# Optimization experiments

Hardware: AMD Instinct MI355X
Metric: run time of the kernel (lower is better)

Reference implementation:

```python
import jax, jax.numpy as jnp
import numpy as np

EMBED_DIM = 512
NUM_HEADS = 8
HEAD_DIM = EMBED_DIM // NUM_HEADS
EDGE_DIM = 16
B, N = 2, 2048


def setup_inputs() -> dict:
    key = jax.random.key(0)
    ks = jax.random.split(key, 16)
    s = 1.0 / np.sqrt(EMBED_DIM)
    inp = {
        "x": jax.random.normal(ks[0], (B, N, EMBED_DIM), dtype=jnp.float32),
        "adjacency": jax.random.uniform(ks[1], (B, N, N), dtype=jnp.float32),
        # torch.nn.Linear stores weight as (out, in); we keep that convention
        "Wq": jax.random.uniform(ks[2], (EMBED_DIM, EMBED_DIM), minval=-s, maxval=s),
        "bq": jax.random.uniform(ks[3], (EMBED_DIM,), minval=-s, maxval=s),
        "Wk": jax.random.uniform(ks[4], (EMBED_DIM, EMBED_DIM), minval=-s, maxval=s),
        "bk": jax.random.uniform(ks[5], (EMBED_DIM,), minval=-s, maxval=s),
        "Wv": jax.random.uniform(ks[6], (EMBED_DIM, EMBED_DIM), minval=-s, maxval=s),
        "bv": jax.random.uniform(ks[7], (EMBED_DIM,), minval=-s, maxval=s),
        "Wo": jax.random.uniform(ks[8], (EMBED_DIM, EMBED_DIM), minval=-s, maxval=s),
        "bo": jax.random.uniform(ks[9], (EMBED_DIM,), minval=-s, maxval=s),
        # edge MLP: Linear(1 -> edge_dim) then Linear(edge_dim -> num_heads)
        "We1": jax.random.uniform(ks[10], (EDGE_DIM, 1), minval=-1.0, maxval=1.0),
        "be1": jax.random.uniform(ks[11], (EDGE_DIM,), minval=-1.0, maxval=1.0),
        "We2": jax.random.uniform(ks[12], (NUM_HEADS, EDGE_DIM), minval=-0.25, maxval=0.25),
        "be2": jax.random.uniform(ks[13], (NUM_HEADS,), minval=-0.25, maxval=0.25),
        "edge_bias": jnp.zeros((NUM_HEADS,), dtype=jnp.float32),
    }
    return inp


def reference(x, adjacency, Wq, bq, Wk, bk, Wv, bv, Wo, bo, We1, be1, We2, be2, edge_bias):
    b, n, _ = x.shape
    scale = HEAD_DIM ** (-0.5)

    def split_heads(t):  # (b, n, E) -> (b, H, n, d)
        return t.reshape(b, n, NUM_HEADS, HEAD_DIM).transpose(0, 2, 1, 3)

    q = split_heads(x @ Wq.T + bq)
    k = split_heads(x @ Wk.T + bk)
    v = split_heads(x @ Wv.T + bv)

    # (b, H, n, n)
    attn_scores = jnp.einsum('bhid,bhjd->bhij', q, k) * scale

    # edge MLP applied pointwise to each adjacency entry: 1 -> edge_dim -> num_heads
    # hidden: (b, n, n, edge_dim)
    hidden = jax.nn.relu(adjacency[..., None] * We1[:, 0] + be1)
    edge_attn = jnp.einsum('bijE,hE->bhij', hidden, We2) + be2[None, :, None, None]

    boost = adjacency[:, None, :, :] * edge_bias[None, :, None, None]
    attn_scores = attn_scores + edge_attn + boost

    attn_probs = jax.nn.softmax(attn_scores, axis=-1)
    out = jnp.einsum('bhij,bhjd->bhid', attn_probs, v)
    out = out.transpose(0, 2, 1, 3).reshape(b, n, EMBED_DIM)
    out = out @ Wo.T + bo
    return out
```

## Files before the change

### kernel.cpp

```cpp
#include <hip/hip_runtime.h>
#include <stdint.h>


#define SEQ 2048
#define EMB 512
#define NH  8
#define HD  64
#define NB  2
#define L2E 1.4426950408889634f

typedef unsigned int   u32;
typedef unsigned short u16;
typedef u32   u32x4  __attribute__((ext_vector_type(4)));
typedef float f32x4  __attribute__((ext_vector_type(4)));
typedef __bf16 bf16x8 __attribute__((ext_vector_type(8)));

#define MFMA16(a, b, c) __builtin_amdgcn_mfma_f32_16x16x32_bf16((a), (b), (c), 0, 0, 0)

static __device__ __forceinline__ u16 f2bf(float f) {
  return __builtin_bit_cast(u16, (__bf16)f);
}
static __device__ __forceinline__ u32 pack2(float a, float b) {
  return (u32)f2bf(a) | ((u32)f2bf(b) << 16);
}
static __device__ __forceinline__ bf16x8 ldfrag(const u16* p) {
  return __builtin_bit_cast(bf16x8, *(const u32x4*)p);
}
static __device__ __forceinline__ void glds16(const u16* g, u16* l) {
  __builtin_amdgcn_global_load_lds(
      (const __attribute__((address_space(1))) u32*)(const void*)g,
      (__attribute__((address_space(3))) u32*)(void*)l, 16, 0, 0);
}


__global__ void prep_kernel(const float* __restrict__ x,
                            const float* __restrict__ Wq, const float* __restrict__ Wk,
                            const float* __restrict__ Wv, const float* __restrict__ Wo,
                            const float* __restrict__ We1, const float* __restrict__ be1,
                            const float* __restrict__ We2, const float* __restrict__ be2,
                            const float* __restrict__ ebias,
                            u16* __restrict__ xb, u16* __restrict__ wqkv,
                            u16* __restrict__ wob, float* __restrict__ co) {
  const int blk = blockIdx.x, tid = threadIdx.x;
  if (blk < 2048) {
    int i = (blk * 256 + tid) * 4;
    float4 v = *(const float4*)(x + i);
    *(uint2*)(xb + i) = make_uint2(pack2(v.x, v.y), pack2(v.z, v.w));
  } else if (blk < 3072) {
    int i = ((blk - 2048) * 256 + tid) * 4;
    int m = i >> 18;
    int off = i & 262143;
    const float* src = (m == 0) ? Wq : ((m == 1) ? Wk : ((m == 2) ? Wv : Wo));
    u16* dst = (m < 3) ? (wqkv + (size_t)m * 262144) : wob;
    float4 v = *(const float4*)(src + off);
    *(uint2*)(dst + off) = make_uint2(pack2(v.x, v.y), pack2(v.z, v.w));
  } else {
    const int e = tid & 15, h = tid >> 4;
    if (tid < 128) {
      co[49 + e * 8 + h] = 0.0f;
      if (h == 0) { co[17 + e] = 0.0f; co[33 + e] = 0.0f; }
    }
    __syncthreads();
    if (tid < 128) {
      float w1 = We1[e], b1 = be1[e], w2 = We2[h * 16 + e];
      float u0 = b1, u1 = w1 + b1;
      bool on  = (u0 >= 0.0f) && (u1 >= 0.0f);
      bool off = (u0 <= 0.0f) && (u1 <= 0.0f);
      bool crossing = (!on) && (!off);
      float ca = on ? (w2 * b1) : (crossing ? 0.5f * w2 * b1 : 0.0f);
      float cb = on ? (w2 * w1) : (crossing ? 0.5f * w2 * w1 : 0.0f);
      #pragma unroll
      for (int d = 1; d < 16; d <<= 1) { ca += __shfl_xor(ca, d); cb += __shfl_xor(cb, d); }
      if (e == 0) { co[h] = (be2[h] + ca) * L2E; co[8 + h] = (ebias[h] + cb) * L2E; }
      unsigned long long msk = __ballot(crossing);
      int midx = __popcll(msk & 0xFFFFull & ((1ull << e) - 1ull));
      int mcnt = __popcll(msk & 0xFFFFull);
      if (crossing) {
        co[49 + midx * 8 + h] = 0.5f * w2 * L2E;
        if (h == 0) { co[17 + midx] = w1; co[33 + midx] = b1; }
      }
      if (tid == 0) ((int*)co)[16] = mcnt;
    }
  }
}

#define LDA 40
__global__ __launch_bounds__(256) void gemm_qkv_kernel(
    const u16* __restrict__ A, const u16* __restrict__ Bm,
    const float* __restrict__ bq, const float* __restrict__ bk, const float* __restrict__ bv,
    u16* __restrict__ qh, u16* __restrict__ ksw, u16* __restrict__ vsw)
{
  __shared__ u16 sm[64 * LDA + 128 * LDA];
  u16* As = sm;
  u16* Bs = sm + 64 * LDA;
  const int tid = threadIdx.x;
  const int lane = tid & 63, w = tid >> 6;
  const int q = lane >> 4, l15 = lane & 15;
  const int m0 = blockIdx.y * 64;
  const int n0 = blockIdx.x * 128;

  f32x4 acc[4][2];
  f32x4 zero = {0.f, 0.f, 0.f, 0.f};
  #pragma unroll
  for (int i = 0; i < 4; i++) { acc[i][0] = zero; acc[i][1] = zero; }

  const bool isA = tid < 128;
  const int arow_ = tid >> 1, ahalf = tid & 1;
  const int brow = tid - 128;
  const u16* ga = A  + (size_t)(m0 + arow_) * EMB + ahalf * 16;
  const u16* gb = Bm + (size_t)(n0 + brow) * EMB;
  u16* la = &As[arow_ * LDA + ahalf * 16];
  u16* lb = &Bs[brow * LDA];

  u32x4 p0, p1, p2, p3;
  if (isA) {
    p0 = *(const u32x4*)(ga); p1 = *(const u32x4*)(ga + 8); ga += 32;
  } else {
    p0 = *(const u32x4*)(gb);      p1 = *(const u32x4*)(gb + 8);
    p2 = *(const u32x4*)(gb + 16); p3 = *(const u32x4*)(gb + 24); gb += 32;
  }

  for (int k0 = 0; k0 < EMB; k0 += 32) {
    __syncthreads();
    if (isA) { *(u32x4*)(la) = p0; *(u32x4*)(la + 8) = p1; }
    else {
      *(u32x4*)(lb)      = p0; *(u32x4*)(lb + 8)  = p1;
      *(u32x4*)(lb + 16) = p2; *(u32x4*)(lb + 24) = p3;
    }
    __syncthreads();
    if (k0 + 32 < EMB) {
      if (isA) { p0 = *(const u32x4*)(ga); p1 = *(const u32x4*)(ga + 8); ga += 32; }
      else {
        p0 = *(const u32x4*)(gb);      p1 = *(const u32x4*)(gb + 8);
        p2 = *(const u32x4*)(gb + 16); p3 = *(const u32x4*)(gb + 24); gb += 32;
      }
    }
    bf16x8 af[4], bfr[2];
    #pragma unroll
    for (int mi = 0; mi < 4; mi++)
      af[mi] = ldfrag(&As[(mi*16 + l15) * LDA + q*8]);
    #pragma unroll
    for (int ni = 0; ni < 2; ni++)
      bfr[ni] = ldfrag(&Bs[(w*32 + ni*16 + l15) * LDA + q*8]);
    #pragma unroll
    for (int mi = 0; mi < 4; mi++)
      #pragma unroll
      for (int ni = 0; ni < 2; ni++)
        acc[mi][ni] = MFMA16(af[mi], bfr[ni], acc[mi][ni]);
  }

  const int mat = n0 >> 9;
  const float* bias = (mat == 0) ? bq : ((mat == 1) ? bk : bv);
  const float mul = (mat == 0) ? 0.125f * L2E : 1.0f;
  const int b_ = m0 >> 11;
  const int nbase = m0 & 2047;

  #pragma unroll
  for (int p = 0; p < 2; p++) {
    __syncthreads();
    if ((w >> 1) == p) {
      #pragma unroll
      for (int ni = 0; ni < 2; ni++) {
        const int dd = (w & 1) * 32 + ni * 16 + l15;
        const float bsv = bias[(n0 & 511) + (w * 32 + ni * 16 + l15)];
        #pragma unroll
        for (int mi = 0; mi < 4; mi++) {
          #pragma unroll
          for (int r = 0; r < 4; r++) {
            const int nr = mi * 16 + q * 4 + r;
            const float val = (acc[mi][ni][r] + bsv) * mul;
            int idx;
            if (mat == 0)      idx = nr * 64 + dd;
            else if (mat == 1) idx = (nr >> 4) * 1024 + ((dd >> 5) << 9)
                                   + ((((dd >> 3) & 3) * 16 + (nr & 15)) << 3) + (dd & 7);
            else               idx = ((dd >> 4) << 10) + (((nr >> 5) & 1) << 9)
                                   + ((((nr >> 3) & 3) * 16 + (dd & 15)) << 3) + (nr & 7);
            sm[idx] = f2bf(val);
          }
        }
      }
    }
    __syncthreads();
    const int hh = ((n0 & 511) >> 6) + p;
    u16* gdst;
    if (mat == 0)      gdst = qh  + ((size_t)(b_ * NH + hh) * SEQ + nbase) * HD;
    else if (mat == 1) gdst = ksw + (size_t)(b_ * NH + hh) * 131072 + (nbase >> 4) * 1024;
    else               gdst = vsw + (size_t)(b_ * NH + hh) * 131072 + (nbase >> 6) * 4096;
    *(u32x4*)(gdst + tid * 16)     = *(const u32x4*)(sm + tid * 16);
    *(u32x4*)(gdst + tid * 16 + 8) = *(const u32x4*)(sm + tid * 16 + 8);
  }
}

__global__ __launch_bounds__(256) void gemm_out_kernel(
    const u16* __restrict__ A, const u16* __restrict__ Bm,
    const float* __restrict__ bo, float* __restrict__ out)
{
  __shared__ u16 As[64 * LDA];
  __shared__ u16 Bs[64 * LDA];
  const int tid = threadIdx.x;
  const int lane = tid & 63, w = tid >> 6;
  const int q = lane >> 4, l15 = lane & 15;
  const int m0 = blockIdx.y * 64;
  const int n0 = blockIdx.x * 64;

  f32x4 acc[4];
  f32x4 zero = {0.f, 0.f, 0.f, 0.f};
  #pragma unroll
  for (int i = 0; i < 4; i++) acc[i] = zero;

  const bool isA = tid < 128;
  const int row = isA ? (tid >> 1) : ((tid - 128) >> 1);
  const int half = tid & 1;
  const u16* g = (isA ? A + (size_t)(m0 + row) * EMB : Bm + (size_t)(n0 + row) * EMB)
               + half * 16;
  u16* l = (isA ? &As[row * LDA] : &Bs[row * LDA]) + half * 16;

  u32x4 p0 = *(const u32x4*)(g);
  u32x4 p1 = *(const u32x4*)(g + 8);
  g += 32;

  for (int k0 = 0; k0 < EMB; k0 += 32) {
    __syncthreads();
    *(u32x4*)(l) = p0; *(u32x4*)(l + 8) = p1;
    __syncthreads();
    if (k0 + 32 < EMB) {
      p0 = *(const u32x4*)(g); p1 = *(const u32x4*)(g + 8); g += 32;
    }
    bf16x8 af[4], bfr;
    #pragma unroll
    for (int mi = 0; mi < 4; mi++)
      af[mi] = ldfrag(&As[(mi*16 + l15) * LDA + q*8]);
    bfr = ldfrag(&Bs[(w*16 + l15) * LDA + q*8]);
    #pragma unroll
    for (int mi = 0; mi < 4; mi++)
      acc[mi] = MFMA16(af[mi], bfr, acc[mi]);
  }

  int col = n0 + w*16 + l15;
  float bsv = bo[col];
  #pragma unroll
  for (int mi = 0; mi < 4; mi++) {
    int rowb = m0 + mi*16 + q*4;
    #pragma unroll
    for (int r = 0; r < 4; r++)
      out[(size_t)(rowb + r) * EMB + col] = acc[mi][r] + bsv;
  }
}

template<int MT>
struct FlashCtx {
  const u16 *kgp, *vgp;
  const float* arow;
  bf16x8 qf0, qf1;
  float Ah, Bh;
  float ctr[MT], dtr[MT], wtr[MT];
  int lane, w, q, l15;
};

template<int MT>
static __device__ __forceinline__ void flash_stage(const FlashCtx<MT>& c,
                                                   u16* Kb, u16* Vb, int it) {
  const int o = c.w * 1024 + c.lane * 8;
  const u16* kg = c.kgp + it * 4096;
  const u16* vg = c.vgp + it * 4096;
  glds16(kg + o,       Kb + o);
  glds16(kg + o + 512, Kb + o + 512);
  glds16(vg + o,       Vb + o);
  glds16(vg + o + 512, Vb + o + 512);
}

template<int MT>
static __device__ __forceinline__ void flash_iter(
    const FlashCtx<MT>& c, int it, u16* Kb, u16* Vb, u16* nKb, u16* nVb,
    u16* psw, float4* avc, float4* avn, f32x4* O, float& lsum)
{
  __syncthreads();
  if (it + 1 < 32) flash_stage(c, nKb, nVb, it + 1);
  const int nx = (it + 1 < 32) ? it + 1 : 31;
  #pragma unroll
  for (int jt = 0; jt < 4; jt++)
    avn[jt] = *(const float4*)(c.arow + nx * 64 + jt * 16);
  __builtin_amdgcn_sched_barrier(0);

  f32x4 zero = {0.f, 0.f, 0.f, 0.f};
  const int lo = c.lane * 8;

  f32x4 S[4];
  #pragma unroll
  for (int jt = 0; jt < 4; jt++) {
    bf16x8 kf0 = ldfrag(Kb + jt * 1024 + lo);
    bf16x8 kf1 = ldfrag(Kb + jt * 1024 + 512 + lo);
    f32x4 s = MFMA16(kf0, c.qf0, zero);
    S[jt] = MFMA16(kf1, c.qf1, s);
  }

  #pragma unroll
  for (int half = 0; half < 2; half++) {
    #pragma unroll
    for (int jj = 0; jj < 2; jj++) {
      const int jt = half * 2 + jj;
      float p[4];
      #pragma unroll
      for (int r = 0; r < 4; r++) {
        float a = ((const float*)&avc[jt])[r];
        float e = fmaf(a, c.Bh, c.Ah);
        #pragma unroll
        for (int t = 0; t < MT; t++)
          e = fmaf(fabsf(fmaf(a, c.ctr[t], c.dtr[t])), c.wtr[t], e);
        p[r] = __builtin_amdgcn_exp2f(S[jt][r] + e);
        lsum += p[r];
      }
      *(uint2*)(psw + c.l15 * 72 + jt * 16 + c.q * 4) =
          make_uint2(pack2(p[0], p[1]), pack2(p[2], p[3]));
    }
    bf16x8 pf = ldfrag(psw + c.l15 * 72 + half * 32 + c.q * 8);
    #pragma unroll
    for (int dt = 0; dt < 4; dt++) {
      bf16x8 vf = ldfrag(Vb + dt * 1024 + half * 512 + lo);
      O[dt] = MFMA16(vf, pf, O[dt]);
    }
  }
}

template<int MT>
__device__ __forceinline__ void flash_body(
    u16* Kb0, u16* Kb1, u16* Vb0, u16* Vb1, u16* Pb,
    const u16* __restrict__ qh, const u16* __restrict__ ksw, const u16* __restrict__ vsw,
    const float* __restrict__ adj, const float* __restrict__ coeff, u16* __restrict__ om)
{
  const int tid = threadIdx.x, lane = tid & 63, w = tid >> 6;
  const int q = lane >> 4, l15 = lane & 15;
  const int i0 = blockIdx.x * 64;
  const int h = blockIdx.y, b = blockIdx.z;
  const int bh = b * NH + h;
  const int iw = i0 + w * 16;

  FlashCtx<MT> c;
  c.lane = lane; c.w = w; c.q = q; c.l15 = l15;
  c.Ah = coeff[h]; c.Bh = coeff[8 + h];
  #pragma unroll
  for (int t = 0; t < MT; t++) {
    c.ctr[t] = coeff[17 + t];
    c.dtr[t] = coeff[33 + t];
    c.wtr[t] = coeff[49 + t * 8 + h];
  }
  const u16* qrow = qh + ((size_t)bh * SEQ + iw + l15) * HD;
  c.qf0 = ldfrag(qrow + q * 8);
  c.qf1 = ldfrag(qrow + 32 + q * 8);
  c.kgp = ksw + (size_t)bh * 131072;
  c.vgp = vsw + (size_t)bh * 131072;
  c.arow = adj + ((size_t)b * SEQ + iw + l15) * SEQ + q * 4;

  f32x4 O[4];
  f32x4 zero = {0.f, 0.f, 0.f, 0.f};
  #pragma unroll
  for (int dt = 0; dt < 4; dt++) O[dt] = zero;
  float lsum = 0.0f;

  u16* psw = Pb + w * 1152;

  flash_stage(c, Kb0, Vb0, 0);
  float4 avA[4], avB[4];
  #pragma unroll
  for (int jt = 0; jt < 4; jt++)
    avA[jt] = *(const float4*)(c.arow + jt * 16);

  #pragma unroll 1
  for (int it2 = 0; it2 < 32; it2 += 2) {
    flash_iter(c, it2,     Kb0, Vb0, Kb1, Vb1, psw, avA, avB, O, lsum);
    flash_iter(c, it2 + 1, Kb1, Vb1, Kb0, Vb0, psw, avB, avA, O, lsum);
  }

  lsum += __shfl_xor(lsum, 16);
  lsum += __shfl_xor(lsum, 32);
  float rl = 1.0f / lsum;

  u16* orow = om + ((size_t)b * SEQ + iw + l15) * EMB + h * HD + q * 4;
  #pragma unroll
  for (int dt = 0; dt < 4; dt++) {
    float v0 = O[dt][0] * rl, v1 = O[dt][1] * rl;
    float v2 = O[dt][2] * rl, v3 = O[dt][3] * rl;
    *(uint2*)(orow + dt * 16) = make_uint2(pack2(v0, v1), pack2(v2, v3));
  }
}

__global__ __launch_bounds__(256, 3) void flash_kernel(
    const u16* __restrict__ qh, const u16* __restrict__ ksw, const u16* __restrict__ vsw,
    const float* __restrict__ adj, const float* __restrict__ coeff, u16* __restrict__ om)
{
  __shared__ __align__(16) u16 Kb[2][4096];
  __shared__ __align__(16) u16 Vb[2][4096];
  __shared__ __align__(16) u16 Pb[4608];
  const int mt = ((const int*)coeff)[16];
  if (mt <= 4)
    flash_body<4>(Kb[0], Kb[1], Vb[0], Vb[1], Pb, qh, ksw, vsw, adj, coeff, om);
  else if (mt <= 8)
    flash_body<8>(Kb[0], Kb[1], Vb[0], Vb[1], Pb, qh, ksw, vsw, adj, coeff, om);
  else
    flash_body<16>(Kb[0], Kb[1], Vb[0], Vb[1], Pb, qh, ksw, vsw, adj, coeff, om);
}

extern "C" void kernel_launch(void* const* d_in, const int* in_sizes, int n_in,
                              void* d_out, int out_size, void* d_ws, size_t ws_size,
                              hipStream_t stream) {
  const float* x     = (const float*)d_in[0];
  const float* adj   = (const float*)d_in[1];
  const float* Wq    = (const float*)d_in[2];
  const float* bq    = (const float*)d_in[3];
  const float* Wk    = (const float*)d_in[4];
  const float* bk    = (const float*)d_in[5];
  const float* Wv    = (const float*)d_in[6];
  const float* bv    = (const float*)d_in[7];
  const float* Wo    = (const float*)d_in[8];
  const float* bo    = (const float*)d_in[9];
  const float* We1   = (const float*)d_in[10];
  const float* be1   = (const float*)d_in[11];
  const float* We2   = (const float*)d_in[12];
  const float* be2   = (const float*)d_in[13];
  const float* ebias = (const float*)d_in[14];
  float* out = (float*)d_out;

  char* ws = (char*)d_ws;
  u16*   xb   = (u16*)(ws + 0);
  u16*   wqkv = (u16*)(ws + 4194304);
  u16*   wob  = (u16*)(ws + 5767168);
  u16*   qh   = (u16*)(ws + 6291456);
  u16*   ksw  = (u16*)(ws + 10485760);
  u16*   vsw  = (u16*)(ws + 14680064);
  u16*   om   = (u16*)(ws + 18874368);
  float* co   = (float*)(ws + 23068672);
  if (ws_size < 23069696) return;

  prep_kernel<<<3073, 256, 0, stream>>>(x, Wq, Wk, Wv, Wo, We1, be1, We2, be2, ebias,
                                        xb, wqkv, wob, co);
  gemm_qkv_kernel<<<dim3(12, 64), 256, 0, stream>>>(xb, wqkv, bq, bk, bv, qh, ksw, vsw);
  flash_kernel<<<dim3(32, NH, NB), 256, 0, stream>>>(qh, ksw, vsw, adj, co, om);
  gemm_out_kernel<<<dim3(8, 64), 256, 0, stream>>>(om, wob, bo, out);
}
```

Measured before the change: 193.3 us.

## Pre-convert adjacency to fp16 in MFMA-fragment order for flash kernel

Adds a prep pass that transposes 16-row adjacency tiles through shared memory and stores them as fp16 in a layout matching the attention fragment order. The flash kernel then loads 8-byte fp16 packets instead of 16-byte fp32 rows, halving adjacency traffic across the eight heads that each re-read it. This costs an extra full read of the fp32 adjacency, a 16 MB write and more workspace, and reduces adjacency precision to fp16.

```diff
diff --git a/kernel.cpp b/kernel.cpp
--- a/kernel.cpp
+++ b/kernel.cpp
@@ -14,6 +14,7 @@
 typedef u32   u32x4  __attribute__((ext_vector_type(4)));
 typedef float f32x4  __attribute__((ext_vector_type(4)));
 typedef __bf16 bf16x8 __attribute__((ext_vector_type(8)));
+typedef _Float16 f16x4 __attribute__((ext_vector_type(4)));
 
 #define MFMA16(a, b, c) __builtin_amdgcn_mfma_f32_16x16x32_bf16((a), (b), (c), 0, 0, 0)
 
@@ -22,6 +23,9 @@
 }
 static __device__ __forceinline__ u32 pack2(float a, float b) {
   return (u32)f2bf(a) | ((u32)f2bf(b) << 16);
+}
+static __device__ __forceinline__ u16 f2h(float f) {
+  return __builtin_bit_cast(u16, (_Float16)f);
 }
 static __device__ __forceinline__ bf16x8 ldfrag(const u16* p) {
   return __builtin_bit_cast(bf16x8, *(const u32x4*)p);
@@ -33,14 +37,16 @@
 }
 
 
-__global__ void prep_kernel(const float* __restrict__ x,
+__global__ void prep_kernel(const float* __restrict__ x, const float* __restrict__ adj,
                             const float* __restrict__ Wq, const float* __restrict__ Wk,
                             const float* __restrict__ Wv, const float* __restrict__ Wo,
                             const float* __restrict__ We1, const float* __restrict__ be1,
                             const float* __restrict__ We2, const float* __restrict__ be2,
                             const float* __restrict__ ebias,
                             u16* __restrict__ xb, u16* __restrict__ wqkv,
-                            u16* __restrict__ wob, float* __restrict__ co) {
+                            u16* __restrict__ wob, float* __restrict__ co,
+                            u16* __restrict__ at) {
+  __shared__ float Ts[16 * 72];
   const int blk = blockIdx.x, tid = threadIdx.x;
   if (blk < 2048) {
     int i = (blk * 256 + tid) * 4;
@@ -54,7 +60,7 @@
     u16* dst = (m < 3) ? (wqkv + (size_t)m * 262144) : wob;
     float4 v = *(const float4*)(src + off);
     *(uint2*)(dst + off) = make_uint2(pack2(v.x, v.y), pack2(v.z, v.w));
-  } else {
+  } else if (blk == 3072) {
     const int e = tid & 15, h = tid >> 4;
     if (tid < 128) {
       co[49 + e * 8 + h] = 0.0f;
@@ -80,6 +86,26 @@
         if (h == 0) { co[17 + midx] = w1; co[33 + midx] = b1; }
       }
       if (tid == 0) ((int*)co)[16] = mcnt;
+    }
+  } else {
+    const int blk2 = blk - 3073;
+    const int b = blk2 >> 7, it16 = blk2 & 127;
+    const float* src = adj + ((size_t)b * SEQ + it16 * 16) * SEQ;
+    u16* dst = at + (size_t)b * 4194304 + (size_t)it16 * 32768;
+    const int row = tid >> 4, jl = tid & 15;
+    const int jq = tid >> 4, il = tid & 15;
+    for (int jc = 0; jc < SEQ; jc += 64) {
+      float4 v = *(const float4*)(src + (size_t)row * SEQ + jc + jl * 4);
+      __syncthreads();
+      *(float4*)&Ts[row * 72 + jl * 4] = v;
+      __syncthreads();
+      float a0 = Ts[il * 72 + jq * 4 + 0];
+      float a1 = Ts[il * 72 + jq * 4 + 1];
+      float a2 = Ts[il * 72 + jq * 4 + 2];
+      float a3 = Ts[il * 72 + jq * 4 + 3];
+      uint2 w2v = make_uint2((u32)f2h(a0) | ((u32)f2h(a1) << 16),
+                             (u32)f2h(a2) | ((u32)f2h(a3) << 16));
+      *(uint2*)(dst + (((jc >> 2) + jq) << 6) + il * 4) = w2v;
     }
   }
 }
@@ -250,7 +276,7 @@
 template<int MT>
 struct FlashCtx {
   const u16 *kgp, *vgp;
-  const float* arow;
+  const u16* aq;
   bf16x8 qf0, qf1;
   float Ah, Bh;
   float ctr[MT], dtr[MT], wtr[MT];
@@ -272,14 +298,14 @@
 template<int MT>
 static __device__ __forceinline__ void flash_iter(
     const FlashCtx<MT>& c, int it, u16* Kb, u16* Vb, u16* nKb, u16* nVb,
-    u16* psw, float4* avc, float4* avn, f32x4* O, float& lsum)
+    u16* psw, uint2* avc, uint2* avn, f32x4* O, float& lsum)
 {
   __syncthreads();
   if (it + 1 < 32) flash_stage(c, nKb, nVb, it + 1);
   const int nx = (it + 1 < 32) ? it + 1 : 31;
   #pragma unroll
   for (int jt = 0; jt < 4; jt++)
-    avn[jt] = *(const float4*)(c.arow + nx * 64 + jt * 16);
+    avn[jt] = *(const uint2*)(c.aq + ((nx * 16 + jt * 4) << 6));
   __builtin_amdgcn_sched_barrier(0);
 
   f32x4 zero = {0.f, 0.f, 0.f, 0.f};
@@ -299,10 +325,11 @@
     #pragma unroll
     for (int jj = 0; jj < 2; jj++) {
       const int jt = half * 2 + jj;
+      f16x4 hv = __builtin_bit_cast(f16x4, avc[jt]);
       float p[4];
       #pragma unroll
       for (int r = 0; r < 4; r++) {
-        float a = ((const float*)&avc[jt])[r];
+        float a = (float)hv[r];
         float e = fmaf(a, c.Bh, c.Ah);
         #pragma unroll
         for (int t = 0; t < MT; t++)
@@ -326,7 +353,7 @@
 __device__ __forceinline__ void flash_body(
     u16* Kb0, u16* Kb1, u16* Vb0, u16* Vb1, u16* Pb,
     const u16* __restrict__ qh, const u16* __restrict__ ksw, const u16* __restrict__ vsw,
-    const float* __restrict__ adj, const float* __restrict__ coeff, u16* __restrict__ om)
+    const u16* __restrict__ at, const float* __restrict__ coeff, u16* __restrict__ om)
 {
   const int tid = threadIdx.x, lane = tid & 63, w = tid >> 6;
   const int q = lane >> 4, l15 = lane & 15;
@@ -349,7 +376,7 @@
   c.qf1 = ldfrag(qrow + 32 + q * 8);
   c.kgp = ksw + (size_t)bh * 131072;
   c.vgp = vsw + (size_t)bh * 131072;
-  c.arow = adj + ((size_t)b * SEQ + iw + l15) * SEQ + q * 4;
+  c.aq  = at + (size_t)b * 4194304 + (size_t)(iw >> 4) * 32768 + q * 64 + l15 * 4;
 
   f32x4 O[4];
   f32x4 zero = {0.f, 0.f, 0.f, 0.f};
@@ -360,10 +387,10 @@
   u16* psw = Pb + w * 1152;
 
   flash_stage(c, Kb0, Vb0, 0);
-  float4 avA[4], avB[4];
+  uint2 avA[4], avB[4];
   #pragma unroll
   for (int jt = 0; jt < 4; jt++)
-    avA[jt] = *(const float4*)(c.arow + jt * 16);
+    avA[jt] = *(const uint2*)(c.aq + ((jt * 4) << 6));
 
   #pragma unroll 1
   for (int it2 = 0; it2 < 32; it2 += 2) {
@@ -386,18 +413,18 @@
 
 __global__ __launch_bounds__(256, 3) void flash_kernel(
     const u16* __restrict__ qh, const u16* __restrict__ ksw, const u16* __restrict__ vsw,
-    const float* __restrict__ adj, const float* __restrict__ coeff, u16* __restrict__ om)
+    const u16* __restrict__ at, const float* __restrict__ coeff, u16* __restrict__ om)
 {
   __shared__ __align__(16) u16 Kb[2][4096];
   __shared__ __align__(16) u16 Vb[2][4096];
   __shared__ __align__(16) u16 Pb[4608];
   const int mt = ((const int*)coeff)[16];
   if (mt <= 4)
-    flash_body<4>(Kb[0], Kb[1], Vb[0], Vb[1], Pb, qh, ksw, vsw, adj, coeff, om);
+    flash_body<4>(Kb[0], Kb[1], Vb[0], Vb[1], Pb, qh, ksw, vsw, at, coeff, om);
   else if (mt <= 8)
-    flash_body<8>(Kb[0], Kb[1], Vb[0], Vb[1], Pb, qh, ksw, vsw, adj, coeff, om);
+    flash_body<8>(Kb[0], Kb[1], Vb[0], Vb[1], Pb, qh, ksw, vsw, at, coeff, om);
   else
-    flash_body<16>(Kb[0], Kb[1], Vb[0], Vb[1], Pb, qh, ksw, vsw, adj, coeff, om);
+    flash_body<16>(Kb[0], Kb[1], Vb[0], Vb[1], Pb, qh, ksw, vsw, at, coeff, om);
 }
 
 extern "C" void kernel_launch(void* const* d_in, const int* in_sizes, int n_in,
@@ -429,11 +456,12 @@
   u16*   vsw  = (u16*)(ws + 14680064);
   u16*   om   = (u16*)(ws + 18874368);
   float* co   = (float*)(ws + 23068672);
-  if (ws_size < 23069696) return;
-
-  prep_kernel<<<3073, 256, 0, stream>>>(x, Wq, Wk, Wv, Wo, We1, be1, We2, be2, ebias,
-                                        xb, wqkv, wob, co);
+  u16*   at   = (u16*)(ws + 23072768);
+  if (ws_size < 39849984) return;
+
+  prep_kernel<<<3329, 256, 0, stream>>>(x, adj, Wq, Wk, Wv, Wo, We1, be1, We2, be2,
+                                        ebias, xb, wqkv, wob, co, at);
   gemm_qkv_kernel<<<dim3(12, 64), 256, 0, stream>>>(xb, wqkv, bq, bk, bv, qh, ksw, vsw);
-  flash_kernel<<<dim3(32, NH, NB), 256, 0, stream>>>(qh, ksw, vsw, adj, co, om);
+  flash_kernel<<<dim3(32, NH, NB), 256, 0, stream>>>(qh, ksw, vsw, at, co, om);
   gemm_out_kernel<<<dim3(8, 64), 256, 0, stream>>>(om, wob, bo, out);
 }
```

After: 214.4 us. 1.11x slower.
